# Performance work log

Measured on AMD Instinct MI355X. Metric: run time of the kernel, lower is better.

## Reference

```python
import jax, jax.numpy as jnp
import numpy as np

B, T, H, V = 256, 128, 256, 50257
H2 = 2 * H


def _lstm_cell(x, h, c, Wih, Whh, bih, bhh):
    # PyTorch LSTMCell: gates = x@Wih^T + bih + h@Whh^T + bhh, split [i, f, g, o]
    g = x @ Wih.T + bih + h @ Whh.T + bhh
    i, f, gc, o = jnp.split(g, 4, axis=-1)
    c2 = jax.nn.sigmoid(f) * c + jax.nn.sigmoid(i) * jnp.tanh(gc)
    h2 = jax.nn.sigmoid(o) * jnp.tanh(c2)
    return h2, c2


def setup_inputs() -> dict:
    key = jax.random.key(0)
    ks = iter(jax.random.split(key, 48))

    def mat(shape, scale):
        return jax.random.normal(next(ks), shape, jnp.float32) * scale

    def xav(shape):
        bound = float(np.sqrt(6.0 / (shape[0] + shape[1])))
        return jax.random.uniform(next(ks), shape, jnp.float32, -bound, bound)

    s, s2 = 1.0 / np.sqrt(H), 1.0 / np.sqrt(H2)
    emb = mat((V, H), 0.02).at[0].set(0.0)  # padding_idx=0
    inp = {
        'x': jax.random.randint(next(ks), (B, T), 0, V, dtype=jnp.int32),
        'emb': emb,
        # bidirectional cells (input H, hidden H)
        'Wih_f': mat((4 * H, H), s), 'Whh_f': mat((4 * H, H), s), 'bih_f': mat((4 * H,), s), 'bhh_f': mat((4 * H,), s),
        'Wih_b': mat((4 * H, H), s), 'Whh_b': mat((4 * H, H), s), 'bih_b': mat((4 * H,), s), 'bhh_b': mat((4 * H,), s),
        # 3 stacked cells (input 2H, hidden 2H)
        'W1ih': mat((4 * H2, H2), s2), 'W1hh': mat((4 * H2, H2), s2), 'b1ih': mat((4 * H2,), s2), 'b1hh': mat((4 * H2,), s2),
        'W2ih': mat((4 * H2, H2), s2), 'W2hh': mat((4 * H2, H2), s2), 'b2ih': mat((4 * H2,), s2), 'b2hh': mat((4 * H2,), s2),
        'W3ih': mat((4 * H2, H2), s2), 'W3hh': mat((4 * H2, H2), s2), 'b3ih': mat((4 * H2,), s2), 'b3hh': mat((4 * H2,), s2),
        # output projection
        'Wout': mat((V, H2), s2), 'bout': mat((V,), s2),
        # xavier-uniform initial states, exactly as the torch forward creates them
        'h0f': xav((B, H)), 'c0f': xav((B, H)), 'h0b': xav((B, H)), 'c0b': xav((B, H)),
        'h01': xav((B, H2)), 'c01': xav((B, H2)), 'h02': xav((B, H2)), 'c02': xav((B, H2)),
        'h03': xav((B, H2)), 'c03': xav((B, H2)),
    }
    return inp


def reference(x, emb, Wih_f, Whh_f, bih_f, bhh_f, Wih_b, Whh_b, bih_b, bhh_b,
              W1ih, W1hh, b1ih, b1hh, W2ih, W2hh, b2ih, b2hh, W3ih, W3hh, b3ih, b3hh,
              Wout, bout, h0f, c0f, h0b, c0b, h01, c01, h02, c02, h03, c03):
    # embedding then .view(T, B, -1) -- a reshape, NOT a transpose (faithful to original)
    seq = emb[x].reshape(T, x.shape[0], H)  # (T, B, H)

    def fstep(carry, xt):
        h, c = _lstm_cell(xt, carry[0], carry[1], Wih_f, Whh_f, bih_f, bhh_f)
        return (h, c), h

    _, fwd = jax.lax.scan(fstep, (h0f, c0f), seq)  # (T, B, H)

    def bstep(carry, xt):
        h, c = _lstm_cell(xt, carry[0], carry[1], Wih_b, Whh_b, bih_b, bhh_b)
        return (h, c), h

    _, bwd = jax.lax.scan(bstep, (h0b, c0b), seq[::-1])  # emitted in processing order == original backward list

    pairs = jnp.concatenate([fwd, bwd], axis=-1)  # (T, B, 2H), matches zip(forward, backward)

    def sstep(carry, xt):
        h1, c1, h2, c2, h3, c3 = carry
        h1, c1 = _lstm_cell(xt, h1, c1, W1ih, W1hh, b1ih, b1hh)
        h2, c2 = _lstm_cell(h1, h2, c2, W2ih, W2hh, b2ih, b2hh)
        # dropout (eval mode) = identity
        h3, c3 = _lstm_cell(h2, h3, c3, W3ih, W3hh, b3ih, b3hh)
        return (h1, c1, h2, c2, h3, c3), None

    (h1, c1, h2, c2, h3, c3), _ = jax.lax.scan(sstep, (h01, c01, h02, c02, h03, c03), pairs)
    return h3 @ Wout.T + bout  # (B, V)
```

## Files before the change

kernel.cpp:

```cpp
#include <hip/hip_runtime.h>


typedef __bf16 bf16x8 __attribute__((ext_vector_type(8)));
typedef __bf16 bf16x4v __attribute__((ext_vector_type(4)));
typedef float f32x4 __attribute__((ext_vector_type(4)));

__device__ __forceinline__ float sigm(float x) { return 1.0f / (1.0f + expf(-x)); }

__device__ __forceinline__ void split8(const f32x4& a0, const f32x4& a1, bf16x8& h,
                                       bf16x8& l) {
#pragma unroll
  for (int j = 0; j < 4; ++j) {
    float f = a0[j];
    __bf16 hb = (__bf16)f;
    h[j] = hb;
    l[j] = (__bf16)(f - (float)hb);
  }
#pragma unroll
  for (int j = 0; j < 4; ++j) {
    float f = a1[j];
    __bf16 hb = (__bf16)f;
    h[4 + j] = hb;
    l[4 + j] = (__bf16)(f - (float)hb);
  }
}

__device__ __forceinline__ void glds16(const void* g, void* l) {
  __builtin_amdgcn_global_load_lds(
      (const __attribute__((address_space(1))) unsigned int*)g,
      (__attribute__((address_space(3))) unsigned int*)l, 16, 0, 0);
}

__global__ __launch_bounds__(256) void k_init(const float* c0f, const float* c0b,
                                              const float* c01, const float* c02,
                                              const float* c03, float* cf, float* cb,
                                              float* c1, float* c2, float* c3) {
  const int i = blockIdx.x * 256 + threadIdx.x;
  if (i < 65536) cf[i] = c0f[i];
  else if (i < 131072) cb[i - 65536] = c0b[i - 65536];
  else if (i < 262144) c1[i - 131072] = c01[i - 131072];
  else if (i < 393216) c2[i - 262144] = c02[i - 262144];
  else c3[i - 393216] = c03[i - 393216];
}

template <int Kx, int Hc>
__device__ __forceinline__ void cell_core(const float* __restrict__ arow,
                                          const float* __restrict__ hrow,
                                          const float* __restrict__ wihrow,
                                          const float* __restrict__ whhrow,
                                          const float* __restrict__ bih,
                                          const float* __restrict__ bhh,
                                          float* __restrict__ cst,
                                          float* __restrict__ ho, int ldho, int m0,
                                          int j0, __bf16* lAh, __bf16* lAl,
                                          __bf16* lBh, __bf16* lBl) {
  const int tid = threadIdx.x, lane = tid & 63, wv = tid >> 6;
  const int mr = lane & 15, qk = (lane >> 4) * 8;
  const int srow = tid >> 2, scq = (tid & 3) * 8;
  constexpr int NX = Kx / 32, NT = NX + Hc / 32;

// ... 146 lines not shown
  const int srow = tid >> 2, scq = (tid & 3) * 8;
  const int m0 = mt * 64;
  int wr = n0 + srow;
  if (wr > 50256) wr = 50256;
  f32x4 acc[4] = {};
  f32x4 a0 = *(const f32x4*)(h3 + (size_t)(m0 + srow) * 512 + scq);
  f32x4 a1 = *(const f32x4*)(h3 + (size_t)(m0 + srow) * 512 + scq + 4);
  f32x4 b0 = *(const f32x4*)(Wt + (size_t)wr * 512 + scq);
  f32x4 b1 = *(const f32x4*)(Wt + (size_t)wr * 512 + scq + 4);
  for (int k = 0; k < 16; ++k) {
    __syncthreads();
    bf16x8 hh, ll;
    split8(a0, a1, hh, ll);
    *(bf16x8*)(sAh + srow * 40 + scq) = hh;
    *(bf16x8*)(sAl + srow * 40 + scq) = ll;
    split8(b0, b1, hh, ll);
    *(bf16x8*)(sBh + srow * 40 + scq) = hh;
    *(bf16x8*)(sBl + srow * 40 + scq) = ll;
    if (k < 15) {
      const int kk = (k + 1) * 32;
      a0 = *(const f32x4*)(h3 + (size_t)(m0 + srow) * 512 + kk + scq);
      a1 = *(const f32x4*)(h3 + (size_t)(m0 + srow) * 512 + kk + scq + 4);
      b0 = *(const f32x4*)(Wt + (size_t)wr * 512 + kk + scq);
      b1 = *(const f32x4*)(Wt + (size_t)wr * 512 + kk + scq + 4);
    }
    __syncthreads();
    bf16x8 ah = *(const bf16x8*)(sAh + (wv * 16 + mr) * 40 + qk);
    bf16x8 al = *(const bf16x8*)(sAl + (wv * 16 + mr) * 40 + qk);
#pragma unroll
    for (int G = 0; G < 4; ++G) {
      bf16x8 bh = *(const bf16x8*)(sBh + (G * 16 + mr) * 40 + qk);
      bf16x8 bl = *(const bf16x8*)(sBl + (G * 16 + mr) * 40 + qk);
      acc[G] = __builtin_amdgcn_mfma_f32_16x16x32_bf16(ah, bh, acc[G], 0, 0, 0);
      acc[G] = __builtin_amdgcn_mfma_f32_16x16x32_bf16(ah, bl, acc[G], 0, 0, 0);
      acc[G] = __builtin_amdgcn_mfma_f32_16x16x32_bf16(al, bh, acc[G], 0, 0, 0);
    }
  }
  const int r0 = (lane >> 4) * 4;
#pragma unroll
  for (int G = 0; G < 4; ++G) {
    const int n = n0 + G * 16 + mr;
    if (n < 50257) {
      const float bv = bo[n];
#pragma unroll
      for (int r = 0; r < 4; ++r) {
        const int brow = m0 + wv * 16 + r0 + r;
        out[(size_t)brow * 50257 + n] = acc[G][r] + bv;
      }
    }
  }
}


struct SJ { const float* s; __bf16* h; __bf16* l; };
struct SplitJobs { SJ j[15]; int pre[16]; };

__global__ __launch_bounds__(256) void k_split(SplitJobs sj) {
  const int e0 = blockIdx.x * 1024;
  int ji = 0;
  while (e0 >= sj.pre[ji + 1]) ++ji;
  const int off = e0 - sj.pre[ji] + threadIdx.x * 4;
  const SJ J = sj.j[ji];
  f32x4 v = *(const f32x4*)(J.s + off);
  bf16x4v h4, l4;
#pragma unroll
  for (int c = 0; c < 4; ++c) {
    __bf16 hb = (__bf16)v[c];
    h4[c] = hb;
    l4[c] = (__bf16)(v[c] - (float)hb);
  }
  *(bf16x4v*)(J.h + off) = h4;
  *(bf16x4v*)(J.l + off) = l4;
}

__global__ __launch_bounds__(256) void k_seqsplit(const int* __restrict__ x,
                                                  const float* __restrict__ emb,
                                                  __bf16* __restrict__ sh,
                                                  __bf16* __restrict__ sl) {
  const int i = (blockIdx.x * 256 + threadIdx.x) * 4;
  const int row = i >> 8;
  const int tok = x[row];
  f32x4 v = *(const f32x4*)(emb + (size_t)tok * 256 + (i & 255));
  bf16x4v h4, l4;
#pragma unroll
  for (int c = 0; c < 4; ++c) {
    __bf16 hb = (__bf16)v[c];
    h4[c] = hb;
    l4[c] = (__bf16)(v[c] - (float)hb);
  }
  *(bf16x4v*)(sh + i) = h4;
  *(bf16x4v*)(sl + i) = l4;
}

template <int KX, int HC>
__device__ __forceinline__ void cell2(
    const __bf16* __restrict__ xh, const __bf16* __restrict__ xl, const int xst,
    const __bf16* __restrict__ hh, const __bf16* __restrict__ hl, const int hst,
    const __bf16* __restrict__ wxh, const __bf16* __restrict__ wxl,
    const __bf16* __restrict__ whh, const __bf16* __restrict__ whl,
    const float* __restrict__ bih, const float* __restrict__ bhh,
    float* __restrict__ cst, __bf16* __restrict__ ohh, __bf16* __restrict__ ohl,
    const int ost, float* __restrict__ of32, const int m0, const int j0,
    __bf16* sm) {
  const int tid = threadIdx.x, lane = tid & 63, wv = tid >> 6;
  const int mr = lane & 15, q8 = (lane >> 4) * 8;
  const int srow = lane >> 2, cbe = (lane & 3) * 8;
  constexpr int NX = KX / 32, NT = NX + HC / 32;
  const int mh = wv & 1, gh = wv >> 1;

  const size_t arow = (size_t)(m0 + wv * 16 + srow);
  const size_t brow = (size_t)(wv * HC + j0 + srow);
  const __bf16* axh = xh + arow * xst + cbe;
  const __bf16* axl = xl + arow * xst + cbe;
  const __bf16* ahh = hh + arow * hst + cbe;
  const __bf16* ahl = hl + arow * hst + cbe;
  const __bf16* bxh = wxh + brow * KX + cbe;
  const __bf16* bxl = wxl + brow * KX + cbe;
  const __bf16* bhh2 = whh + brow * HC + cbe;
  const __bf16* bhl2 = whl + brow * HC + cbe;

  auto issue = [&](int kb, int bbuf) {
    const bool xp = kb < NX;
    const int ko = (xp ? kb : kb - NX) * 32;
    __bf16* d = sm + bbuf * 8192 + wv * 512;
    glds16((xp ? axh : ahh) + ko, d);
    glds16((xp ? axl : ahl) + ko, d + 2048);
    glds16((xp ? bxh : bhh2) + ko, d + 4096);
    glds16((xp ? bxl : bhl2) + ko, d + 6144);
  };

  f32x4 acc[2][2] = {};
  issue(0, 0);
  int bb = 0;
  for (int kb = 0; kb < NT; ++kb) {
    const int nb = (bb == 2) ? 0 : bb + 1;
    if (kb + 1 < NT) {
      issue(kb + 1, nb);
      asm volatile("s_waitcnt vmcnt(4)" ::: "memory");
    } else {
      asm volatile("s_waitcnt vmcnt(0)" ::: "memory");
    }
    __builtin_amdgcn_s_barrier();
    asm volatile("" ::: "memory");
    const __bf16* base = sm + bb * 8192;
    bf16x8 fah[2], fal[2], fbh[2], fbl[2];
#pragma unroll
    for (int i = 0; i < 2; ++i) {
      const int ra = ((2 * mh + i) * 16 + mr) * 32 + q8;
      const int rb = ((2 * gh + i) * 16 + mr) * 32 + q8;
      fah[i] = *(const bf16x8*)(base + ra);
      fal[i] = *(const bf16x8*)(base + 2048 + ra);
      fbh[i] = *(const bf16x8*)(base + 4096 + rb);
      fbl[i] = *(const bf16x8*)(base + 6144 + rb);
    }
#pragma unroll
    for (int am = 0; am < 2; ++am)
#pragma unroll
      for (int ag = 0; ag < 2; ++ag) {
        acc[am][ag] =
            __builtin_amdgcn_mfma_f32_16x16x32_bf16(fah[am], fbh[ag], acc[am][ag], 0, 0, 0);
        acc[am][ag] =
            __builtin_amdgcn_mfma_f32_16x16x32_bf16(fah[am], fbl[ag], acc[am][ag], 0, 0, 0);
        acc[am][ag] =
            __builtin_amdgcn_mfma_f32_16x16x32_bf16(fal[am], fbh[ag], acc[am][ag], 0, 0, 0);
      }
    bb = nb;
  }

  __syncthreads();
  float* gb = (float*)sm;
  {
    const int r0 = (lane >> 4) * 4;
#pragma unroll
    for (int am = 0; am < 2; ++am)
#pragma unroll
      for (int ag = 0; ag < 2; ++ag) {
        const int g = 2 * gh + ag;
        const int rowb = (2 * mh + am) * 16 + r0;
#pragma unroll
        for (int r = 0; r < 4; ++r)
          gb[(g * 64 + rowb + r) * 20 + mr] = acc[am][ag][r];
      }
  }
  __syncthreads();
  const int row = tid >> 2, c0 = (tid & 3) * 4, jc = j0 + c0;
  f32x4 gi = *(const f32x4*)(gb + (0 * 64 + row) * 20 + c0);
  f32x4 gf = *(const f32x4*)(gb + (1 * 64 + row) * 20 + c0);
  f32x4 gg = *(const f32x4*)(gb + (2 * 64 + row) * 20 + c0);
  f32x4 go = *(const f32x4*)(gb + (3 * 64 + row) * 20 + c0);
  f32x4 bI = *(const f32x4*)(bih + jc) + *(const f32x4*)(bhh + jc);
  f32x4 bF = *(const f32x4*)(bih + HC + jc) + *(const f32x4*)(bhh + HC + jc);
  f32x4 bG = *(const f32x4*)(bih + 2 * HC + jc) + *(const f32x4*)(bhh + 2 * HC + jc);
  f32x4 bO = *(const f32x4*)(bih + 3 * HC + jc) + *(const f32x4*)(bhh + 3 * HC + jc);
  const size_t ci = (size_t)(m0 + row) * HC + jc;
  f32x4 cc = *(f32x4*)(cst + ci);
  f32x4 hn;
  bf16x4v h4, l4;
#pragma unroll
  for (int c = 0; c < 4; ++c) {
    const float I = sigm(gi[c] + bI[c]);
    const float F = sigm(gf[c] + bF[c]);
    const float G = tanhf(gg[c] + bG[c]);
    const float O = sigm(go[c] + bO[c]);
    const float cn = F * cc[c] + I * G;
    cc[c] = cn;
    const float hv = O * tanhf(cn);
    hn[c] = hv;
    const __bf16 hb = (__bf16)hv;
    h4[c] = hb;
    l4[c] = (__bf16)(hv - (float)hb);
  }
  *(f32x4*)(cst + ci) = cc;
  *(bf16x4v*)(ohh + (size_t)(m0 + row) * ost + jc) = h4;
  *(bf16x4v*)(ohl + (size_t)(m0 + row) * ost + jc) = l4;
  if (of32) *(f32x4*)(of32 + (size_t)(m0 + row) * HC + jc) = hn;
}

struct P2 {
  const __bf16 *seqh, *seql;
  const __bf16 *Wfh, *Wfl, *Ufh, *Ufl;
  const __bf16 *Wbh, *Wbl, *Ubh, *Ubl;
  const __bf16 *W1h, *W1l, *U1h, *U1l;
  const __bf16 *W2h, *W2l, *U2h, *U2l;
  const __bf16 *W3h, *W3l, *U3h, *U3l;
  const float *bihf, *bhhf, *bihb, *bhhb;
  const float *b1ih, *b1hh, *b2ih, *b2hh, *b3ih, *b3hh;
  const __bf16 *h0fh, *h0fl, *h0bh, *h0bl;
  const __bf16 *h01h, *h01l, *h02h, *h02l, *h03h, *h03l;
  __bf16 *prh, *prl, *h1h, *h1l, *h2h, *h2l, *h3h, *h3l;
  float *cf, *cb, *c1, *c2, *c3;
  float* h3f;
};

__global__ __launch_bounds__(256) void k_step2(P2 p, int s) {
  __shared__ __align__(16) __bf16 sm[3 * 4 * 2048];
  const int wg = blockIdx.x;
  const int RING = 256 * 512;
  if (wg < 128) {
    const int dir = wg >> 6, widx = wg & 63, t = s;
    if (t >= 128) return;
    const int m0 = (widx >> 4) * 64, j0 = (widx & 15) * 16;
    const int tt = dir ? 127 - t : t;
    const __bf16* xh = p.seqh + (size_t)tt * 65536;
    const __bf16* xl = p.seql + (size_t)tt * 65536;
    const __bf16 *hh, *hl;
    int hst;
    if (t == 0) {
      hh = dir ? p.h0bh : p.h0fh;
      hl = dir ? p.h0bl : p.h0fl;
      hst = 256;
    } else {
      const size_t off = (size_t)((t - 1) & 3) * RING + (dir ? 256 : 0);
      hh = p.prh + off;
      hl = p.prl + off;
      hst = 512;
    }
    const size_t oo = (size_t)(t & 3) * RING + (dir ? 256 : 0);
    cell2<256, 256>(xh, xl, 256, hh, hl, hst, dir ? p.Wbh : p.Wfh,
                    dir ? p.Wbl : p.Wfl, dir ? p.Ubh : p.Ufh, dir ? p.Ubl : p.Ufl,
                    dir ? p.bihb : p.bihf, dir ? p.bhhb : p.bhhf,
                    dir ? p.cb : p.cf, p.prh + oo, p.prl + oo, 512, nullptr, m0, j0,
                    sm);
  } else {
    const int st = (wg - 128) >> 7;
    const int widx = (wg - 128) & 127;
    const int t = s - 1 - st;
    if (t < 0 || t >= 128) return;
    const int m0 = (widx >> 5) * 64, j0 = (widx & 31) * 16;
    const size_t ring = (size_t)(t & 3) * RING, ringp = (size_t)((t - 1) & 3) * RING;
    const __bf16 *xh, *xl, *hh, *hl, *wxh, *wxl, *whh, *whl;
    const float *bi, *bh2;
    float* cst;
    float* of = nullptr;
    __bf16 *oh, *ol;
    if (st == 0) {
      xh = p.prh + ring; xl = p.prl + ring;
      if (t == 0) { hh = p.h01h; hl = p.h01l; } else { hh = p.h1h + ringp; hl = p.h1l + ringp; }
      wxh = p.W1h; wxl = p.W1l; whh = p.U1h; whl = p.U1l;
      bi = p.b1ih; bh2 = p.b1hh; cst = p.c1; oh = p.h1h + ring; ol = p.h1l + ring;
    } else if (st == 1) {
      xh = p.h1h + ring; xl = p.h1l + ring;
      if (t == 0) { hh = p.h02h; hl = p.h02l; } else { hh = p.h2h + ringp; hl = p.h2l + ringp; }
      wxh = p.W2h; wxl = p.W2l; whh = p.U2h; whl = p.U2l;
      bi = p.b2ih; bh2 = p.b2hh; cst = p.c2; oh = p.h2h + ring; ol = p.h2l + ring;
    } else {
      xh = p.h2h + ring; xl = p.h2l + ring;
      if (t == 0) { hh = p.h03h; hl = p.h03l; } else { hh = p.h3h + ringp; hl = p.h3l + ringp; }
      wxh = p.W3h; wxl = p.W3l; whh = p.U3h; whl = p.U3l;
      bi = p.b3ih; bh2 = p.b3hh; cst = p.c3; oh = p.h3h + ring; ol = p.h3l + ring;
      if (t == 127) of = p.h3f;
    }
    cell2<512, 512>(xh, xl, 512, hh, hl, 512, wxh, wxl, whh, whl, bi, bh2, cst, oh,
                    ol, 512, of, m0, j0, sm);
  }
}

extern "C" void kernel_launch(void* const* d_in, const int* in_sizes, int n_in,
                              void* d_out, int out_size, void* d_ws, size_t ws_size,
                              hipStream_t stream) {
  (void)in_sizes; (void)n_in; (void)out_size;

  const size_t MB = 1ull << 20;
  const bool packA = ws_size >= 44 * MB;
  const bool packB = !packA && ws_size >= 31 * MB;

  if (packA || packB) {
    char* pw = (char*)d_ws;
    char* po = (char*)d_out;
    auto tw = [&](size_t n) { char* r = pw; pw += (n + 255) & ~(size_t)255; return r; };
    auto to = [&](size_t n) { char* r = po; po += (n + 255) & ~(size_t)255; return r; };

    float* h3f = (float*)tw(512 * 1024);
    __bf16* seqh = (__bf16*)to(16 * MB);
    __bf16* seql = (__bf16*)to(16 * MB);

    const size_t WSM = 524288, WBG = 2097152;
    __bf16 *Wfh = (__bf16*)tw(WSM), *Wfl = (__bf16*)tw(WSM);
    __bf16 *Ufh = (__bf16*)tw(WSM), *Ufl = (__bf16*)tw(WSM);
    __bf16 *Wbh = (__bf16*)tw(WSM), *Wbl = (__bf16*)tw(WSM);
    __bf16 *Ubh = (__bf16*)tw(WSM), *Ubl = (__bf16*)tw(WSM);
    __bf16 *W1h = (__bf16*)tw(WBG), *W1l = (__bf16*)tw(WBG);
    __bf16 *U1h = (__bf16*)tw(WBG), *U1l = (__bf16*)tw(WBG);
    __bf16 *W2h = (__bf16*)tw(WBG), *W2l = (__bf16*)tw(WBG);
    __bf16 *U2h = (__bf16*)tw(WBG), *U2l = (__bf16*)tw(WBG);
    __bf16 *W3h = (__bf16*)tw(WBG), *W3l = (__bf16*)tw(WBG);
    __bf16 *U3h = (__bf16*)tw(WBG), *U3l = (__bf16*)tw(WBG);

    auto tr = [&](size_t n) { return packA ? tw(n) : to(n); };
    __bf16* h0fh = (__bf16*)tr(131072);
    __bf16* h0fl = (__bf16*)tr(131072);
    __bf16* h0bh = (__bf16*)tr(131072);
    __bf16* h0bl = (__bf16*)tr(131072);
    __bf16* h01h = (__bf16*)tr(262144);
    __bf16* h01l = (__bf16*)tr(262144);
    __bf16* h02h = (__bf16*)tr(262144);
    __bf16* h02l = (__bf16*)tr(262144);
    __bf16* h03h = (__bf16*)tr(262144);
    __bf16* h03l = (__bf16*)tr(262144);
    const size_t RB = 4ull * 131072 * 2;
    __bf16* prh = (__bf16*)tr(RB);
    __bf16* prl = (__bf16*)tr(RB);
    __bf16* h1h = (__bf16*)tr(RB);
    __bf16* h1l = (__bf16*)tr(RB);
    __bf16* h2h = (__bf16*)tr(RB);
    __bf16* h2l = (__bf16*)tr(RB);
    __bf16* h3h = (__bf16*)tr(RB);
    __bf16* h3l = (__bf16*)tr(RB);
    float* cf = (float*)tr(262144);
    float* cb = (float*)tr(262144);
    float* c1 = (float*)tr(524288);
    float* c2 = (float*)tr(524288);
    float* c3 = (float*)tr(524288);

    SplitJobs sj;
    int np = 0, pre = 0;
    auto addj = [&](const void* s, __bf16* h, __bf16* l, int n) {
      sj.j[np].s = (const float*)s; sj.j[np].h = h; sj.j[np].l = l;
      sj.pre[np] = pre; pre += n; ++np;
    };
    addj(d_in[2], Wfh, Wfl, 262144);
    addj(d_in[3], Ufh, Ufl, 262144);
    addj(d_in[6], Wbh, Wbl, 262144);
    addj(d_in[7], Ubh, Ubl, 262144);
    addj(d_in[10], W1h, W1l, 1048576);
    addj(d_in[11], U1h, U1l, 1048576);
    addj(d_in[14], W2h, W2l, 1048576);
    addj(d_in[15], U2h, U2l, 1048576);
    addj(d_in[18], W3h, W3l, 1048576);
    addj(d_in[19], U3h, U3l, 1048576);
    addj(d_in[24], h0fh, h0fl, 65536);
    addj(d_in[26], h0bh, h0bl, 65536);
    addj(d_in[28], h01h, h01l, 131072);
    addj(d_in[30], h02h, h02l, 131072);
    addj(d_in[32], h03h, h03l, 131072);
    sj.pre[np] = pre;

    P2 p;
    p.seqh = seqh; p.seql = seql;
    p.Wfh = Wfh; p.Wfl = Wfl; p.Ufh = Ufh; p.Ufl = Ufl;
    p.Wbh = Wbh; p.Wbl = Wbl; p.Ubh = Ubh; p.Ubl = Ubl;
    p.W1h = W1h; p.W1l = W1l; p.U1h = U1h; p.U1l = U1l;
    p.W2h = W2h; p.W2l = W2l; p.U2h = U2h; p.U2l = U2l;
    p.W3h = W3h; p.W3l = W3l; p.U3h = U3h; p.U3l = U3l;
    p.bihf = (const float*)d_in[4]; p.bhhf = (const float*)d_in[5];
    p.bihb = (const float*)d_in[8]; p.bhhb = (const float*)d_in[9];
    p.b1ih = (const float*)d_in[12]; p.b1hh = (const float*)d_in[13];
    p.b2ih = (const float*)d_in[16]; p.b2hh = (const float*)d_in[17];
    p.b3ih = (const float*)d_in[20]; p.b3hh = (const float*)d_in[21];
    p.h0fh = h0fh; p.h0fl = h0fl; p.h0bh = h0bh; p.h0bl = h0bl;
    p.h01h = h01h; p.h01l = h01l; p.h02h = h02h; p.h02l = h02l;
    p.h03h = h03h; p.h03l = h03l;
    p.prh = prh; p.prl = prl; p.h1h = h1h; p.h1l = h1l;
    p.h2h = h2h; p.h2l = h2l; p.h3h = h3h; p.h3l = h3l;
    p.cf = cf; p.cb = cb; p.c1 = c1; p.c2 = c2; p.c3 = c3;
    p.h3f = h3f;

    k_split<<<dim3(7680), dim3(256), 0, stream>>>(sj);
    k_seqsplit<<<dim3(8192), dim3(256), 0, stream>>>((const int*)d_in[0],
                                                     (const float*)d_in[1], seqh, seql);
    k_init<<<dim3(2048), dim3(256), 0, stream>>>(
        (const float*)d_in[25], (const float*)d_in[27], (const float*)d_in[29],
        (const float*)d_in[31], (const float*)d_in[33], cf, cb, c1, c2, c3);

    for (int s = 0; s < 131; ++s)
      k_step2<<<dim3(512), dim3(256), 0, stream>>>(p, s);

    k_out<<<dim3(3144), dim3(256), 0, stream>>>(h3f, (const float*)d_in[22],
                                                (const float*)d_in[23], (float*)d_out);
    return;
  }

  char* wsp = (char*)d_ws;
  float* h3c = (float*)wsp;

  const size_t SMALL = 1ull << 19, BIG = 11ull << 20;
  char* w = (ws_size >= SMALL + BIG + (1ull << 20)) ? wsp + SMALL : (char*)d_out;
  auto take = [&](size_t bytes) {
    char* r = w;
    w += (bytes + 255) & ~(size_t)255;
    return r;
  };
  float* pairs = (float*)take(4ull * 256 * 512 * 4);
  float* h1a = (float*)take(4ull * 256 * 512 * 4);
  float* h2a = (float*)take(4ull * 256 * 512 * 4);
  float* h3a = (float*)take(4ull * 256 * 512 * 4);
  float* cf = (float*)take(256ull * 256 * 4);
  float* cb = (float*)take(256ull * 256 * 4);
  float* c1 = (float*)take(256ull * 512 * 4);
  float* c2 = (float*)take(256ull * 512 * 4);
  float* c3 = (float*)take(256ull * 512 * 4);

  P p;
  p.x = (const int*)d_in[0];
  p.emb = (const float*)d_in[1];
  p.pairs = pairs; p.h1a = h1a; p.h2a = h2a; p.h3a = h3a;
  p.cf = cf; p.cb = cb; p.c1 = c1; p.c2 = c2; p.c3 = c3;
  p.Wihf = (const float*)d_in[2];  p.Whhf = (const float*)d_in[3];
  p.bihf = (const float*)d_in[4];  p.bhhf = (const float*)d_in[5];
  p.Wihb = (const float*)d_in[6];  p.Whhb = (const float*)d_in[7];
  p.bihb = (const float*)d_in[8];  p.bhhb = (const float*)d_in[9];
  p.W1ih = (const float*)d_in[10]; p.W1hh = (const float*)d_in[11];
  p.b1ih = (const float*)d_in[12]; p.b1hh = (const float*)d_in[13];
  p.W2ih = (const float*)d_in[14]; p.W2hh = (const float*)d_in[15];
  p.b2ih = (const float*)d_in[16]; p.b2hh = (const float*)d_in[17];
  p.W3ih = (const float*)d_in[18]; p.W3hh = (const float*)d_in[19];
  p.b3ih = (const float*)d_in[20]; p.b3hh = (const float*)d_in[21];
  const float* Wout = (const float*)d_in[22];
  const float* bout = (const float*)d_in[23];
  p.h0f = (const float*)d_in[24]; p.h0b = (const float*)d_in[26];
  p.h01 = (const float*)d_in[28]; p.h02 = (const float*)d_in[30];
  p.h03 = (const float*)d_in[32];

  k_init<<<dim3(2048), dim3(256), 0, stream>>>(
      (const float*)d_in[25], (const float*)d_in[27], (const float*)d_in[29],
      (const float*)d_in[31], (const float*)d_in[33], cf, cb, c1, c2, c3);

  for (int s = 0; s < 131; ++s)
    k_step<<<dim3(512), dim3(256), 0, stream>>>(p, s);
// ... 5 lines not shown
```

Measured before the change: 3.157 ms.

## Widen LSTM step tiles to 32 hidden columns with 5-stage prefetch pipeline

Each workgroup in the per-timestep LSTM kernel now computes 64 rows by 32 hidden units per gate instead of 16, which halves the grid from 512 to 256 blocks. Each wave owns one gate and computes a 4x2 grid of MFMA tiles, reusing the A fragments across more output columns. The shared-memory ring grows from 3 to 5 buffers with three K-blocks prefetched ahead, to hide global-load latency. In exchange, per-block LDS use and register pressure go up and fewer blocks run, which may leave CUs idle on a latency-bound recurrence.

```diff
diff --git a/kernel.cpp b/kernel.cpp
--- a/kernel.cpp
+++ b/kernel.cpp
@@ -299,7 +299,7 @@
 }
 
 template <int KX, int HC>
-__device__ __forceinline__ void cell2(
+__device__ __forceinline__ void cellW(
     const __bf16* __restrict__ xh, const __bf16* __restrict__ xl, const int xst,
     const __bf16* __restrict__ hh, const __bf16* __restrict__ hl, const int hst,
     const __bf16* __restrict__ wxh, const __bf16* __restrict__ wxl,
@@ -310,67 +310,90 @@
     __bf16* sm) {
   const int tid = threadIdx.x, lane = tid & 63, wv = tid >> 6;
   const int mr = lane & 15, q8 = (lane >> 4) * 8;
-  const int srow = lane >> 2, cbe = (lane & 3) * 8;
+  const int sr4 = lane >> 2, ch8 = (lane & 3) * 8;
   constexpr int NX = KX / 32, NT = NX + HC / 32;
-  const int mh = wv & 1, gh = wv >> 1;
-
-  const size_t arow = (size_t)(m0 + wv * 16 + srow);
-  const size_t brow = (size_t)(wv * HC + j0 + srow);
-  const __bf16* axh = xh + arow * xst + cbe;
-  const __bf16* axl = xl + arow * xst + cbe;
-  const __bf16* ahh = hh + arow * hst + cbe;
-  const __bf16* ahl = hl + arow * hst + cbe;
-  const __bf16* bxh = wxh + brow * KX + cbe;
-  const __bf16* bxl = wxl + brow * KX + cbe;
-  const __bf16* bhh2 = whh + brow * HC + cbe;
-  const __bf16* bhl2 = whl + brow * HC + cbe;
-
-  auto issue = [&](int kb, int bbuf) {
-    const bool xp = kb < NX;
-    const int ko = (xp ? kb : kb - NX) * 32;
-    __bf16* d = sm + bbuf * 8192 + wv * 512;
-    glds16((xp ? axh : ahh) + ko, d);
-    glds16((xp ? axl : ahl) + ko, d + 2048);
-    glds16((xp ? bxh : bhh2) + ko, d + 4096);
-    glds16((xp ? bxl : bhl2) + ko, d + 6144);
+  constexpr int NB = 5, BSZ = 12288;
+
+  const __bf16* aX = xh + (size_t)(m0 + wv * 16 + sr4) * xst + ch8;
+  const __bf16* aXl = xl + (size_t)(m0 + wv * 16 + sr4) * xst + ch8;
+  const __bf16* aH = hh + (size_t)(m0 + wv * 16 + sr4) * hst + ch8;
+  const __bf16* aHl = hl + (size_t)(m0 + wv * 16 + sr4) * hst + ch8;
+  const int wr0 = wv * HC + j0 + sr4;
+  const __bf16* bX0 = wxh + (size_t)wr0 * KX + ch8;
+  const __bf16* bX1 = wxh + (size_t)(wr0 + 16) * KX + ch8;
+  const __bf16* bXl0 = wxl + (size_t)wr0 * KX + ch8;
+  const __bf16* bXl1 = wxl + (size_t)(wr0 + 16) * KX + ch8;
+  const __bf16* bH0 = whh + (size_t)wr0 * HC + ch8;
+  const __bf16* bH1 = whh + (size_t)(wr0 + 16) * HC + ch8;
+  const __bf16* bHl0 = whl + (size_t)wr0 * HC + ch8;
+  const __bf16* bHl1 = whl + (size_t)(wr0 + 16) * HC + ch8;
+
+  auto issue = [&](int kb, int bf) {
+    __bf16* d = sm + bf * BSZ;
+    if (kb < NX) {
+      const int ko = kb * 32;
+      glds16(aX + ko, d + wv * 512);
+      glds16(aXl + ko, d + 2048 + wv * 512);
+      glds16(bX0 + ko, d + 4096 + wv * 1024);
+      glds16(bX1 + ko, d + 4096 + wv * 1024 + 512);
+      glds16(bXl0 + ko, d + 8192 + wv * 1024);
+      glds16(bXl1 + ko, d + 8192 + wv * 1024 + 512);
+    } else {
+      const int ko = (kb - NX) * 32;
+      glds16(aH + ko, d + wv * 512);
+      glds16(aHl + ko, d + 2048 + wv * 512);
+      glds16(bH0 + ko, d + 4096 + wv * 1024);
+      glds16(bH1 + ko, d + 4096 + wv * 1024 + 512);
+      glds16(bHl0 + ko, d + 8192 + wv * 1024);
+      glds16(bHl1 + ko, d + 8192 + wv * 1024 + 512);
+    }
   };
 
-  f32x4 acc[2][2] = {};
+  f32x4 acc[4][2] = {};
   issue(0, 0);
-  int bb = 0;
+  issue(1, 1);
+  issue(2, 2);
+  int nx = 3, nbf = 3, cbf = 0;
   for (int kb = 0; kb < NT; ++kb) {
-    const int nb = (bb == 2) ? 0 : bb + 1;
-    if (kb + 1 < NT) {
-      issue(kb + 1, nb);
-      asm volatile("s_waitcnt vmcnt(4)" ::: "memory");
+    if (nx < NT) {
+      issue(nx, nbf);
+      ++nx;
+      nbf = (nbf == NB - 1) ? 0 : nbf + 1;
+      asm volatile("s_waitcnt vmcnt(18)" ::: "memory");
     } else {
-      asm volatile("s_waitcnt vmcnt(0)" ::: "memory");
+      const int rem = NT - 1 - kb;
+      if (rem >= 2) asm volatile("s_waitcnt vmcnt(12)" ::: "memory");
+      else if (rem == 1) asm volatile("s_waitcnt vmcnt(6)" ::: "memory");
+      else asm volatile("s_waitcnt vmcnt(0)" ::: "memory");
     }
     __builtin_amdgcn_s_barrier();
     asm volatile("" ::: "memory");
-    const __bf16* base = sm + bb * 8192;
-    bf16x8 fah[2], fal[2], fbh[2], fbl[2];
-#pragma unroll
-    for (int i = 0; i < 2; ++i) {
-      const int ra = ((2 * mh + i) * 16 + mr) * 32 + q8;
-      const int rb = ((2 * gh + i) * 16 + mr) * 32 + q8;
-      fah[i] = *(const bf16x8*)(base + ra);
-      fal[i] = *(const bf16x8*)(base + 2048 + ra);
-      fbh[i] = *(const bf16x8*)(base + 4096 + rb);
-      fbl[i] = *(const bf16x8*)(base + 6144 + rb);
-    }
-#pragma unroll
-    for (int am = 0; am < 2; ++am)
-#pragma unroll
-      for (int ag = 0; ag < 2; ++ag) {
-        acc[am][ag] =
-            __builtin_amdgcn_mfma_f32_16x16x32_bf16(fah[am], fbh[ag], acc[am][ag], 0, 0, 0);
-        acc[am][ag] =
-            __builtin_amdgcn_mfma_f32_16x16x32_bf16(fah[am], fbl[ag], acc[am][ag], 0, 0, 0);
-        acc[am][ag] =
-            __builtin_amdgcn_mfma_f32_16x16x32_bf16(fal[am], fbh[ag], acc[am][ag], 0, 0, 0);
+    const __bf16* base = sm + cbf * BSZ;
+    cbf = (cbf == NB - 1) ? 0 : cbf + 1;
+    bf16x8 fah[4], fal[4], fbh[2], fbl[2];
+#pragma unroll
+    for (int am = 0; am < 4; ++am) {
+      const int ra = (am * 16 + mr) * 32 + q8;
+      fah[am] = *(const bf16x8*)(base + ra);
+      fal[am] = *(const bf16x8*)(base + 2048 + ra);
+    }
+#pragma unroll
+    for (int an = 0; an < 2; ++an) {
+      const int rb = (wv * 32 + an * 16 + mr) * 32 + q8;
+      fbh[an] = *(const bf16x8*)(base + 4096 + rb);
+      fbl[an] = *(const bf16x8*)(base + 8192 + rb);
+    }
+#pragma unroll
+    for (int am = 0; am < 4; ++am)
+#pragma unroll
+      for (int an = 0; an < 2; ++an) {
+        acc[am][an] = __builtin_amdgcn_mfma_f32_16x16x32_bf16(fah[am], fbh[an],
+                                                              acc[am][an], 0, 0, 0);
+        acc[am][an] = __builtin_amdgcn_mfma_f32_16x16x32_bf16(fah[am], fbl[an],
+                                                              acc[am][an], 0, 0, 0);
+        acc[am][an] = __builtin_amdgcn_mfma_f32_16x16x32_bf16(fal[am], fbh[an],
+                                                              acc[am][an], 0, 0, 0);
       }
-    bb = nb;
   }
 
   __syncthreads();
@@ -378,48 +401,65 @@
   {
     const int r0 = (lane >> 4) * 4;
 #pragma unroll
-    for (int am = 0; am < 2; ++am)
-#pragma unroll
-      for (int ag = 0; ag < 2; ++ag) {
-        const int g = 2 * gh + ag;
-        const int rowb = (2 * mh + am) * 16 + r0;
+    for (int am = 0; am < 4; ++am)
+#pragma unroll
+      for (int an = 0; an < 2; ++an)
 #pragma unroll
         for (int r = 0; r < 4; ++r)
-          gb[(g * 64 + rowb + r) * 20 + mr] = acc[am][ag][r];
-      }
+          gb[(wv * 64 + am * 16 + r0 + r) * 40 + an * 16 + mr] = acc[am][an][r];
   }
   __syncthreads();
-  const int row = tid >> 2, c0 = (tid & 3) * 4, jc = j0 + c0;
-  f32x4 gi = *(const f32x4*)(gb + (0 * 64 + row) * 20 + c0);
-  f32x4 gf = *(const f32x4*)(gb + (1 * 64 + row) * 20 + c0);
-  f32x4 gg = *(const f32x4*)(gb + (2 * 64 + row) * 20 + c0);
-  f32x4 go = *(const f32x4*)(gb + (3 * 64 + row) * 20 + c0);
-  f32x4 bI = *(const f32x4*)(bih + jc) + *(const f32x4*)(bhh + jc);
-  f32x4 bF = *(const f32x4*)(bih + HC + jc) + *(const f32x4*)(bhh + HC + jc);
-  f32x4 bG = *(const f32x4*)(bih + 2 * HC + jc) + *(const f32x4*)(bhh + 2 * HC + jc);
-  f32x4 bO = *(const f32x4*)(bih + 3 * HC + jc) + *(const f32x4*)(bhh + 3 * HC + jc);
+  const int row = tid >> 2, c0 = (tid & 3) * 8, jc = j0 + c0;
+  f32x4 g0[4], g1[4];
+#pragma unroll
+  for (int g = 0; g < 4; ++g) {
+    const f32x4 bA = *(const f32x4*)(bih + g * HC + jc) +
+                     *(const f32x4*)(bhh + g * HC + jc);
+    const f32x4 bB = *(const f32x4*)(bih + g * HC + jc + 4) +
+                     *(const f32x4*)(bhh + g * HC + jc + 4);
+    g0[g] = *(const f32x4*)(gb + (g * 64 + row) * 40 + c0) + bA;
+    g1[g] = *(const f32x4*)(gb + (g * 64 + row) * 40 + c0 + 4) + bB;
+  }
   const size_t ci = (size_t)(m0 + row) * HC + jc;
-  f32x4 cc = *(f32x4*)(cst + ci);
-  f32x4 hn;
-  bf16x4v h4, l4;
+  f32x4 cc0 = *(f32x4*)(cst + ci), cc1 = *(f32x4*)(cst + ci + 4);
+  f32x4 hn0, hn1;
+  bf16x8 h8, l8;
 #pragma unroll
   for (int c = 0; c < 4; ++c) {
-    const float I = sigm(gi[c] + bI[c]);
-    const float F = sigm(gf[c] + bF[c]);
-    const float G = tanhf(gg[c] + bG[c]);
-    const float O = sigm(go[c] + bO[c]);
-    const float cn = F * cc[c] + I * G;
-    cc[c] = cn;
+    const float I = sigm(g0[0][c]);
+    const float F = sigm(g0[1][c]);
+    const float G = tanhf(g0[2][c]);
+    const float O = sigm(g0[3][c]);
+    const float cn = F * cc0[c] + I * G;
+    cc0[c] = cn;
     const float hv = O * tanhf(cn);
-    hn[c] = hv;
+    hn0[c] = hv;
     const __bf16 hb = (__bf16)hv;
-    h4[c] = hb;
-    l4[c] = (__bf16)(hv - (float)hb);
-  }
-  *(f32x4*)(cst + ci) = cc;
-  *(bf16x4v*)(ohh + (size_t)(m0 + row) * ost + jc) = h4;
-  *(bf16x4v*)(ohl + (size_t)(m0 + row) * ost + jc) = l4;
-  if (of32) *(f32x4*)(of32 + (size_t)(m0 + row) * HC + jc) = hn;
+    h8[c] = hb;
+    l8[c] = (__bf16)(hv - (float)hb);
+  }
+#pragma unroll
+  for (int c = 0; c < 4; ++c) {
+    const float I = sigm(g1[0][c]);
+    const float F = sigm(g1[1][c]);
+    const float G = tanhf(g1[2][c]);
+    const float O = sigm(g1[3][c]);
+    const float cn = F * cc1[c] + I * G;
+    cc1[c] = cn;
+    const float hv = O * tanhf(cn);
+    hn1[c] = hv;
+    const __bf16 hb = (__bf16)hv;
+    h8[4 + c] = hb;
+    l8[4 + c] = (__bf16)(hv - (float)hb);
+  }
+  *(f32x4*)(cst + ci) = cc0;
+  *(f32x4*)(cst + ci + 4) = cc1;
+  *(bf16x8*)(ohh + (size_t)(m0 + row) * ost + jc) = h8;
+  *(bf16x8*)(ohl + (size_t)(m0 + row) * ost + jc) = l8;
+  if (of32) {
+    *(f32x4*)(of32 + (size_t)(m0 + row) * HC + jc) = hn0;
+    *(f32x4*)(of32 + (size_t)(m0 + row) * HC + jc + 4) = hn1;
+  }
 }
 
 struct P2 {
@@ -438,65 +478,65 @@
   float* h3f;
 };
 
-__global__ __launch_bounds__(256) void k_step2(P2 p, int s) {
-  __shared__ __align__(16) __bf16 sm[3 * 4 * 2048];
+__global__ __launch_bounds__(256) void k_step3(P2 p, int s) {
+  __shared__ __align__(16) __bf16 sm[5 * 12288];
   const int wg = blockIdx.x;
   const int RING = 256 * 512;
-  if (wg < 128) {
-    const int dir = wg >> 6, widx = wg & 63, t = s;
+  if (wg < 64) {
+    const int dir = wg >> 5, widx = wg & 31, t = s;
     if (t >= 128) return;
-    const int m0 = (widx >> 4) * 64, j0 = (widx & 15) * 16;
+    const int m0 = (widx >> 3) * 64, j0 = (widx & 7) * 32;
     const int tt = dir ? 127 - t : t;
     const __bf16* xh = p.seqh + (size_t)tt * 65536;
     const __bf16* xl = p.seql + (size_t)tt * 65536;
-    const __bf16 *hh, *hl;
+    const __bf16 *hhp, *hlp;
     int hst;
     if (t == 0) {
-      hh = dir ? p.h0bh : p.h0fh;
-      hl = dir ? p.h0bl : p.h0fl;
+      hhp = dir ? p.h0bh : p.h0fh;
+      hlp = dir ? p.h0bl : p.h0fl;
       hst = 256;
     } else {
       const size_t off = (size_t)((t - 1) & 3) * RING + (dir ? 256 : 0);
-      hh = p.prh + off;
-      hl = p.prl + off;
+      hhp = p.prh + off;
+      hlp = p.prl + off;
       hst = 512;
     }
     const size_t oo = (size_t)(t & 3) * RING + (dir ? 256 : 0);
-    cell2<256, 256>(xh, xl, 256, hh, hl, hst, dir ? p.Wbh : p.Wfh,
+    cellW<256, 256>(xh, xl, 256, hhp, hlp, hst, dir ? p.Wbh : p.Wfh,
                     dir ? p.Wbl : p.Wfl, dir ? p.Ubh : p.Ufh, dir ? p.Ubl : p.Ufl,
                     dir ? p.bihb : p.bihf, dir ? p.bhhb : p.bhhf,
                     dir ? p.cb : p.cf, p.prh + oo, p.prl + oo, 512, nullptr, m0, j0,
                     sm);
   } else {
-    const int st = (wg - 128) >> 7;
-    const int widx = (wg - 128) & 127;
+    const int st = (wg - 64) >> 6;
+    const int widx = (wg - 64) & 63;
     const int t = s - 1 - st;
     if (t < 0 || t >= 128) return;
-    const int m0 = (widx >> 5) * 64, j0 = (widx & 31) * 16;
+    const int m0 = (widx >> 4) * 64, j0 = (widx & 15) * 32;
     const size_t ring = (size_t)(t & 3) * RING, ringp = (size_t)((t - 1) & 3) * RING;
-    const __bf16 *xh, *xl, *hh, *hl, *wxh, *wxl, *whh, *whl;
+    const __bf16 *xh, *xl, *hhp, *hlp, *wxh, *wxl, *whp, *wlp;
     const float *bi, *bh2;
     float* cst;
     float* of = nullptr;
     __bf16 *oh, *ol;
     if (st == 0) {
       xh = p.prh + ring; xl = p.prl + ring;
-      if (t == 0) { hh = p.h01h; hl = p.h01l; } else { hh = p.h1h + ringp; hl = p.h1l + ringp; }
-      wxh = p.W1h; wxl = p.W1l; whh = p.U1h; whl = p.U1l;
+      if (t == 0) { hhp = p.h01h; hlp = p.h01l; } else { hhp = p.h1h + ringp; hlp = p.h1l + ringp; }
+      wxh = p.W1h; wxl = p.W1l; whp = p.U1h; wlp = p.U1l;
       bi = p.b1ih; bh2 = p.b1hh; cst = p.c1; oh = p.h1h + ring; ol = p.h1l + ring;
     } else if (st == 1) {
       xh = p.h1h + ring; xl = p.h1l + ring;
-      if (t == 0) { hh = p.h02h; hl = p.h02l; } else { hh = p.h2h + ringp; hl = p.h2l + ringp; }
-      wxh = p.W2h; wxl = p.W2l; whh = p.U2h; whl = p.U2l;
+      if (t == 0) { hhp = p.h02h; hlp = p.h02l; } else { hhp = p.h2h + ringp; hlp = p.h2l + ringp; }
+      wxh = p.W2h; wxl = p.W2l; whp = p.U2h; wlp = p.U2l;
       bi = p.b2ih; bh2 = p.b2hh; cst = p.c2; oh = p.h2h + ring; ol = p.h2l + ring;
     } else {
       xh = p.h2h + ring; xl = p.h2l + ring;
-      if (t == 0) { hh = p.h03h; hl = p.h03l; } else { hh = p.h3h + ringp; hl = p.h3l + ringp; }
-      wxh = p.W3h; wxl = p.W3l; whh = p.U3h; whl = p.U3l;
+      if (t == 0) { hhp = p.h03h; hlp = p.h03l; } else { hhp = p.h3h + ringp; hlp = p.h3l + ringp; }
+      wxh = p.W3h; wxl = p.W3l; whp = p.U3h; wlp = p.U3l;
       bi = p.b3ih; bh2 = p.b3hh; cst = p.c3; oh = p.h3h + ring; ol = p.h3l + ring;
       if (t == 127) of = p.h3f;
     }
-    cell2<512, 512>(xh, xl, 512, hh, hl, 512, wxh, wxl, whh, whl, bi, bh2, cst, oh,
+    cellW<512, 512>(xh, xl, 512, hhp, hlp, 512, wxh, wxl, whp, wlp, bi, bh2, cst, oh,
                     ol, 512, of, m0, j0, sm);
   }
 }
@@ -609,7 +649,7 @@
         (const float*)d_in[31], (const float*)d_in[33], cf, cb, c1, c2, c3);
 
     for (int s = 0; s < 131; ++s)
-      k_step2<<<dim3(512), dim3(256), 0, stream>>>(p, s);
+      k_step3<<<dim3(256), dim3(256), 0, stream>>>(p, s);
 
     k_out<<<dim3(3144), dim3(256), 0, stream>>>(h3f, (const float*)d_in[22],
                                                 (const float*)d_in[23], (float*)d_out);
```

New measurement: 9.419 ms. 198% more time.

## Deepen cell GEMM LDS pipeline to four buffers and remap LDS layout

Applied to the files above, without the earlier changes.

The per-step LSTM cell GEMM now keeps two tiles in flight instead of one. It uses a four-slot LDS ring and waits with vmcnt(8). The global-to-LDS load mapping also changes so each lane loads a row segment matching the MFMA fragment layout (kq*128 + mr*8). This should cut bank conflicts and simplify the fragment-read addressing. LDS use grows from three buffers to four, and the deeper prefetch adds register and wait-count bookkeeping.

```diff
diff --git a/kernel.cpp b/kernel.cpp
--- a/kernel.cpp
+++ b/kernel.cpp
@@ -309,51 +309,65 @@
     const int ost, float* __restrict__ of32, const int m0, const int j0,
     __bf16* sm) {
   const int tid = threadIdx.x, lane = tid & 63, wv = tid >> 6;
-  const int mr = lane & 15, q8 = (lane >> 4) * 8;
-  const int srow = lane >> 2, cbe = (lane & 3) * 8;
+  const int mr = lane & 15;
+  const int kq = lane >> 4;
   constexpr int NX = KX / 32, NT = NX + HC / 32;
+  constexpr int BSZ = 8192;
   const int mh = wv & 1, gh = wv >> 1;
 
-  const size_t arow = (size_t)(m0 + wv * 16 + srow);
-  const size_t brow = (size_t)(wv * HC + j0 + srow);
-  const __bf16* axh = xh + arow * xst + cbe;
-  const __bf16* axl = xl + arow * xst + cbe;
-  const __bf16* ahh = hh + arow * hst + cbe;
-  const __bf16* ahl = hl + arow * hst + cbe;
-  const __bf16* bxh = wxh + brow * KX + cbe;
-  const __bf16* bxl = wxl + brow * KX + cbe;
-  const __bf16* bhh2 = whh + brow * HC + cbe;
-  const __bf16* bhl2 = whl + brow * HC + cbe;
-
-  auto issue = [&](int kb, int bbuf) {
-    const bool xp = kb < NX;
-    const int ko = (xp ? kb : kb - NX) * 32;
-    __bf16* d = sm + bbuf * 8192 + wv * 512;
-    glds16((xp ? axh : ahh) + ko, d);
-    glds16((xp ? axl : ahl) + ko, d + 2048);
-    glds16((xp ? bxh : bhh2) + ko, d + 4096);
-    glds16((xp ? bxl : bhl2) + ko, d + 6144);
+  const int kq8 = kq * 8;
+  const __bf16* axh = xh + (size_t)(m0 + wv * 16 + mr) * xst + kq8;
+  const __bf16* axl = xl + (size_t)(m0 + wv * 16 + mr) * xst + kq8;
+  const __bf16* ahh = hh + (size_t)(m0 + wv * 16 + mr) * hst + kq8;
+  const __bf16* ahl = hl + (size_t)(m0 + wv * 16 + mr) * hst + kq8;
+  const int wr = wv * HC + j0 + mr;
+  const __bf16* bxh = wxh + (size_t)wr * KX + kq8;
+  const __bf16* bxl = wxl + (size_t)wr * KX + kq8;
+  const __bf16* bhh2 = whh + (size_t)wr * HC + kq8;
+  const __bf16* bhl2 = whl + (size_t)wr * HC + kq8;
+
+  auto issue = [&](int kb, int bf) {
+    __bf16* d = sm + bf * BSZ + wv * 512;
+    if (kb < NX) {
+      const int ko = kb * 32;
+      glds16(axh + ko, d);
+      glds16(axl + ko, d + 2048);
+      glds16(bxh + ko, d + 4096);
+      glds16(bxl + ko, d + 6144);
+    } else {
+      const int ko = (kb - NX) * 32;
+      glds16(ahh + ko, d);
+      glds16(ahl + ko, d + 2048);
+      glds16(bhh2 + ko, d + 4096);
+      glds16(bhl2 + ko, d + 6144);
+    }
   };
 
   f32x4 acc[2][2] = {};
   issue(0, 0);
-  int bb = 0;
+  issue(1, 1);
+  int cbf = 0, nbf = 2, nx = 2;
   for (int kb = 0; kb < NT; ++kb) {
-    const int nb = (bb == 2) ? 0 : bb + 1;
-    if (kb + 1 < NT) {
-      issue(kb + 1, nb);
+    if (nx < NT) {
+      issue(nx, nbf);
+      ++nx;
+      nbf = (nbf + 1) & 3;
+      asm volatile("s_waitcnt vmcnt(8)" ::: "memory");
+    } else if (kb < NT - 1) {
       asm volatile("s_waitcnt vmcnt(4)" ::: "memory");
     } else {
       asm volatile("s_waitcnt vmcnt(0)" ::: "memory");
     }
     __builtin_amdgcn_s_barrier();
     asm volatile("" ::: "memory");
-    const __bf16* base = sm + bb * 8192;
+    const __bf16* base = sm + cbf * BSZ;
+    cbf = (cbf + 1) & 3;
+    const int ro = kq * 128 + mr * 8;
     bf16x8 fah[2], fal[2], fbh[2], fbl[2];
 #pragma unroll
     for (int i = 0; i < 2; ++i) {
-      const int ra = ((2 * mh + i) * 16 + mr) * 32 + q8;
-      const int rb = ((2 * gh + i) * 16 + mr) * 32 + q8;
+      const int ra = (2 * mh + i) * 512 + ro;
+      const int rb = (2 * gh + i) * 512 + ro;
       fah[i] = *(const bf16x8*)(base + ra);
       fal[i] = *(const bf16x8*)(base + 2048 + ra);
       fbh[i] = *(const bf16x8*)(base + 4096 + rb);
@@ -370,7 +384,6 @@
         acc[am][ag] =
             __builtin_amdgcn_mfma_f32_16x16x32_bf16(fal[am], fbh[ag], acc[am][ag], 0, 0, 0);
       }
-    bb = nb;
   }
 
   __syncthreads();
@@ -439,7 +452,7 @@
 };
 
 __global__ __launch_bounds__(256) void k_step2(P2 p, int s) {
-  __shared__ __align__(16) __bf16 sm[3 * 4 * 2048];
+  __shared__ __align__(16) __bf16 sm[4 * 8192];
   const int wg = blockIdx.x;
   const int RING = 256 * 512;
   if (wg < 128) {
```

Result: slower. 7.814 ms (+147.5%).

## Store split bf16 weights and activations in MFMA-tiled swizzled layout

Applied to the files above, without the earlier changes.

Weights, initial states, embeddings and the per-step hidden outputs are now written in a tiled 16-row by 32-column block layout that matches the MFMA fragment order. Each wave's global-to-LDS load then reads one contiguous 1 KB block instead of 16 strided row segments, and the LDS fragment reads use the same tile order. The goal is more coalesced global loads in the recurrent step kernel. In exchange, every producer and consumer has to agree on the swizzle, so any path still using the old row-major indexing would read wrong data.

```diff
diff --git a/kernel.cpp b/kernel.cpp
--- a/kernel.cpp
+++ b/kernel.cpp
@@ -6,6 +6,11 @@
 typedef float f32x4 __attribute__((ext_vector_type(4)));
 
 __device__ __forceinline__ float sigm(float x) { return 1.0f / (1.0f + expf(-x)); }
+
+__device__ __forceinline__ int swz(int r, int k, int lw) {
+  return ((((r >> 4) << (lw - 5)) + (k >> 5)) << 9) + (((k >> 3) & 3) << 7) +
+         ((r & 15) << 3) + (k & 7);
+}
 
 __device__ __forceinline__ void split8(const f32x4& a0, const f32x4& a1, bf16x8& h,
                                        bf16x8& l) {
@@ -258,7 +263,7 @@
 }
 
 
-struct SJ { const float* s; __bf16* h; __bf16* l; };
+struct SJ { const float* s; __bf16* h; __bf16* l; int lw; };
 struct SplitJobs { SJ j[15]; int pre[16]; };
 
 __global__ __launch_bounds__(256) void k_split(SplitJobs sj) {
@@ -267,6 +272,8 @@
   while (e0 >= sj.pre[ji + 1]) ++ji;
   const int off = e0 - sj.pre[ji] + threadIdx.x * 4;
   const SJ J = sj.j[ji];
+  const int r = off >> J.lw, k = off & ((1 << J.lw) - 1);
+  const int so = swz(r, k, J.lw);
   f32x4 v = *(const f32x4*)(J.s + off);
   bf16x4v h4, l4;
 #pragma unroll
@@ -275,8 +282,8 @@
     h4[c] = hb;
     l4[c] = (__bf16)(v[c] - (float)hb);
   }
-  *(bf16x4v*)(J.h + off) = h4;
-  *(bf16x4v*)(J.l + off) = l4;
+  *(bf16x4v*)(J.h + so) = h4;
+  *(bf16x4v*)(J.l + so) = l4;
 }
 
 __global__ __launch_bounds__(256) void k_seqsplit(const int* __restrict__ x,
@@ -284,9 +291,10 @@
                                                   __bf16* __restrict__ sh,
                                                   __bf16* __restrict__ sl) {
   const int i = (blockIdx.x * 256 + threadIdx.x) * 4;
-  const int row = i >> 8;
+  const int row = i >> 8, k = i & 255;
   const int tok = x[row];
-  f32x4 v = *(const f32x4*)(emb + (size_t)tok * 256 + (i & 255));
+  const int so = swz(row, k, 8);
+  f32x4 v = *(const f32x4*)(emb + (size_t)tok * 256 + k);
   bf16x4v h4, l4;
 #pragma unroll
   for (int c = 0; c < 4; ++c) {
@@ -294,50 +302,60 @@
     h4[c] = hb;
     l4[c] = (__bf16)(v[c] - (float)hb);
   }
-  *(bf16x4v*)(sh + i) = h4;
-  *(bf16x4v*)(sl + i) = l4;
+  *(bf16x4v*)(sh + so) = h4;
+  *(bf16x4v*)(sl + so) = l4;
 }
 
 template <int KX, int HC>
 __device__ __forceinline__ void cell2(
-    const __bf16* __restrict__ xh, const __bf16* __restrict__ xl, const int xst,
-    const __bf16* __restrict__ hh, const __bf16* __restrict__ hl, const int hst,
+    const __bf16* __restrict__ xh, const __bf16* __restrict__ xl, const int xW,
+    const __bf16* __restrict__ hh, const __bf16* __restrict__ hl, const int hW,
+    const int hc0,
     const __bf16* __restrict__ wxh, const __bf16* __restrict__ wxl,
     const __bf16* __restrict__ whh, const __bf16* __restrict__ whl,
     const float* __restrict__ bih, const float* __restrict__ bhh,
     float* __restrict__ cst, __bf16* __restrict__ ohh, __bf16* __restrict__ ohl,
-    const int ost, float* __restrict__ of32, const int m0, const int j0,
+    const int oc0, float* __restrict__ of32, const int m0, const int j0,
     __bf16* sm) {
   const int tid = threadIdx.x, lane = tid & 63, wv = tid >> 6;
-  const int mr = lane & 15, q8 = (lane >> 4) * 8;
-  const int srow = lane >> 2, cbe = (lane & 3) * 8;
+  const int mr = lane & 15, kq = lane >> 4;
   constexpr int NX = KX / 32, NT = NX + HC / 32;
+  constexpr int BSZ = 8192;
   const int mh = wv & 1, gh = wv >> 1;
 
-  const size_t arow = (size_t)(m0 + wv * 16 + srow);
-  const size_t brow = (size_t)(wv * HC + j0 + srow);
-  const __bf16* axh = xh + arow * xst + cbe;
-  const __bf16* axl = xl + arow * xst + cbe;
-  const __bf16* ahh = hh + arow * hst + cbe;
-  const __bf16* ahl = hl + arow * hst + cbe;
-  const __bf16* bxh = wxh + brow * KX + cbe;
-  const __bf16* bxl = wxl + brow * KX + cbe;
-  const __bf16* bhh2 = whh + brow * HC + cbe;
-  const __bf16* bhl2 = whl + brow * HC + cbe;
-
-  auto issue = [&](int kb, int bbuf) {
-    const bool xp = kb < NX;
-    const int ko = (xp ? kb : kb - NX) * 32;
-    __bf16* d = sm + bbuf * 8192 + wv * 512;
-    glds16((xp ? axh : ahh) + ko, d);
-    glds16((xp ? axl : ahl) + ko, d + 2048);
-    glds16((xp ? bxh : bhh2) + ko, d + 4096);
-    glds16((xp ? bxl : bhl2) + ko, d + 6144);
+  const int arg = (m0 >> 4) + wv;
+  const int brg = wv * (HC >> 4) + (j0 >> 4);
+  const int l8 = lane * 8;
+  const __bf16* paxh = xh + (size_t)arg * (xW >> 5) * 512 + l8;
+  const __bf16* paxl = xl + (size_t)arg * (xW >> 5) * 512 + l8;
+  const __bf16* pahh = hh + ((size_t)arg * (hW >> 5) + (hc0 >> 5)) * 512 + l8;
+  const __bf16* pahl = hl + ((size_t)arg * (hW >> 5) + (hc0 >> 5)) * 512 + l8;
+  const __bf16* pbxh = wxh + (size_t)brg * (KX >> 5) * 512 + l8;
+  const __bf16* pbxl = wxl + (size_t)brg * (KX >> 5) * 512 + l8;
+  const __bf16* pbhh = whh + (size_t)brg * (HC >> 5) * 512 + l8;
+  const __bf16* pbhl = whl + (size_t)brg * (HC >> 5) * 512 + l8;
+
+  auto issue = [&](int kb, int bf) {
+    __bf16* d = sm + bf * BSZ + wv * 512;
+    if (kb < NX) {
+      const int ko = kb * 512;
+      glds16(paxh + ko, d);
+      glds16(paxl + ko, d + 2048);
+      glds16(pbxh + ko, d + 4096);
+      glds16(pbxl + ko, d + 6144);
+    } else {
+      const int ko = (kb - NX) * 512;
+      glds16(pahh + ko, d);
+      glds16(pahl + ko, d + 2048);
+      glds16(pbhh + ko, d + 4096);
+      glds16(pbhl + ko, d + 6144);
+    }
   };
 
   f32x4 acc[2][2] = {};
   issue(0, 0);
   int bb = 0;
+  const int ro = kq * 128 + mr * 8;
   for (int kb = 0; kb < NT; ++kb) {
     const int nb = (bb == 2) ? 0 : bb + 1;
     if (kb + 1 < NT) {
@@ -348,12 +366,12 @@
     }
     __builtin_amdgcn_s_barrier();
     asm volatile("" ::: "memory");
-    const __bf16* base = sm + bb * 8192;
+    const __bf16* base = sm + bb * BSZ;
     bf16x8 fah[2], fal[2], fbh[2], fbl[2];
 #pragma unroll
     for (int i = 0; i < 2; ++i) {
-      const int ra = ((2 * mh + i) * 16 + mr) * 32 + q8;
-      const int rb = ((2 * gh + i) * 16 + mr) * 32 + q8;
+      const int ra = (2 * mh + i) * 512 + ro;
+      const int rb = (2 * gh + i) * 512 + ro;
       fah[i] = *(const bf16x8*)(base + ra);
       fal[i] = *(const bf16x8*)(base + 2048 + ra);
       fbh[i] = *(const bf16x8*)(base + 4096 + rb);
@@ -417,8 +435,9 @@
     l4[c] = (__bf16)(hv - (float)hb);
   }
   *(f32x4*)(cst + ci) = cc;
-  *(bf16x4v*)(ohh + (size_t)(m0 + row) * ost + jc) = h4;
-  *(bf16x4v*)(ohl + (size_t)(m0 + row) * ost + jc) = l4;
+  const int so = swz(m0 + row, oc0 + jc, 9);
+  *(bf16x4v*)(ohh + so) = h4;
+  *(bf16x4v*)(ohl + so) = l4;
   if (of32) *(f32x4*)(of32 + (size_t)(m0 + row) * HC + jc) = hn;
 }
 
@@ -439,7 +458,7 @@
 };
 
 __global__ __launch_bounds__(256) void k_step2(P2 p, int s) {
-  __shared__ __align__(16) __bf16 sm[3 * 4 * 2048];
+  __shared__ __align__(16) __bf16 sm[3 * 8192];
   const int wg = blockIdx.x;
   const int RING = 256 * 512;
   if (wg < 128) {
@@ -450,23 +469,23 @@
     const __bf16* xh = p.seqh + (size_t)tt * 65536;
     const __bf16* xl = p.seql + (size_t)tt * 65536;
     const __bf16 *hh, *hl;
-    int hst;
+    int hW, hc0;
     if (t == 0) {
       hh = dir ? p.h0bh : p.h0fh;
       hl = dir ? p.h0bl : p.h0fl;
-      hst = 256;
+      hW = 256; hc0 = 0;
     } else {
-      const size_t off = (size_t)((t - 1) & 3) * RING + (dir ? 256 : 0);
+      const size_t off = (size_t)((t - 1) & 3) * RING;
       hh = p.prh + off;
       hl = p.prl + off;
-      hst = 512;
-    }
-    const size_t oo = (size_t)(t & 3) * RING + (dir ? 256 : 0);
-    cell2<256, 256>(xh, xl, 256, hh, hl, hst, dir ? p.Wbh : p.Wfh,
+      hW = 512; hc0 = dir ? 256 : 0;
+    }
+    const size_t oo = (size_t)(t & 3) * RING;
+    cell2<256, 256>(xh, xl, 256, hh, hl, hW, hc0, dir ? p.Wbh : p.Wfh,
                     dir ? p.Wbl : p.Wfl, dir ? p.Ubh : p.Ufh, dir ? p.Ubl : p.Ufl,
                     dir ? p.bihb : p.bihf, dir ? p.bhhb : p.bhhf,
-                    dir ? p.cb : p.cf, p.prh + oo, p.prl + oo, 512, nullptr, m0, j0,
-                    sm);
+                    dir ? p.cb : p.cf, p.prh + oo, p.prl + oo, dir ? 256 : 0,
+                    nullptr, m0, j0, sm);
   } else {
     const int st = (wg - 128) >> 7;
     const int widx = (wg - 128) & 127;
@@ -496,8 +515,8 @@
       bi = p.b3ih; bh2 = p.b3hh; cst = p.c3; oh = p.h3h + ring; ol = p.h3l + ring;
       if (t == 127) of = p.h3f;
     }
-    cell2<512, 512>(xh, xl, 512, hh, hl, 512, wxh, wxl, whh, whl, bi, bh2, cst, oh,
-                    ol, 512, of, m0, j0, sm);
+    cell2<512, 512>(xh, xl, 512, hh, hl, 512, 0, wxh, wxl, whh, whl, bi, bh2, cst,
+                    oh, ol, 0, of, m0, j0, sm);
   }
 }
 
@@ -560,25 +579,25 @@
 
     SplitJobs sj;
     int np = 0, pre = 0;
-    auto addj = [&](const void* s, __bf16* h, __bf16* l, int n) {
-      sj.j[np].s = (const float*)s; sj.j[np].h = h; sj.j[np].l = l;
+    auto addj = [&](const void* s, __bf16* h, __bf16* l, int n, int lw) {
+      sj.j[np].s = (const float*)s; sj.j[np].h = h; sj.j[np].l = l; sj.j[np].lw = lw;
       sj.pre[np] = pre; pre += n; ++np;
     };
-    addj(d_in[2], Wfh, Wfl, 262144);
-    addj(d_in[3], Ufh, Ufl, 262144);
-    addj(d_in[6], Wbh, Wbl, 262144);
-    addj(d_in[7], Ubh, Ubl, 262144);
-    addj(d_in[10], W1h, W1l, 1048576);
-    addj(d_in[11], U1h, U1l, 1048576);
-    addj(d_in[14], W2h, W2l, 1048576);
-    addj(d_in[15], U2h, U2l, 1048576);
-    addj(d_in[18], W3h, W3l, 1048576);
-    addj(d_in[19], U3h, U3l, 1048576);
-    addj(d_in[24], h0fh, h0fl, 65536);
-    addj(d_in[26], h0bh, h0bl, 65536);
-    addj(d_in[28], h01h, h01l, 131072);
-    addj(d_in[30], h02h, h02l, 131072);
-    addj(d_in[32], h03h, h03l, 131072);
+    addj(d_in[2], Wfh, Wfl, 262144, 8);
+    addj(d_in[3], Ufh, Ufl, 262144, 8);
+    addj(d_in[6], Wbh, Wbl, 262144, 8);
+    addj(d_in[7], Ubh, Ubl, 262144, 8);
+    addj(d_in[10], W1h, W1l, 1048576, 9);
+    addj(d_in[11], U1h, U1l, 1048576, 9);
+    addj(d_in[14], W2h, W2l, 1048576, 9);
+    addj(d_in[15], U2h, U2l, 1048576, 9);
+    addj(d_in[18], W3h, W3l, 1048576, 9);
+    addj(d_in[19], U3h, U3l, 1048576, 9);
+    addj(d_in[24], h0fh, h0fl, 65536, 8);
+    addj(d_in[26], h0bh, h0bl, 65536, 8);
+    addj(d_in[28], h01h, h01l, 131072, 9);
+    addj(d_in[30], h02h, h02l, 131072, 9);
+    addj(d_in[32], h03h, h03l, 131072, 9);
     sj.pre[np] = pre;
 
     P2 p;
```

Result: slower. 6.760 ms (+114.1%).
